# Kernel tuning notes

Hardware: AMD Instinct MI355X
Metric: run time of the kernel (lower is better)

Reference implementation:

```python
import jax, jax.numpy as jnp
import numpy as np

D_MODEL = 512
NUM_HEADS = 8
D_QKV = D_MODEL // NUM_HEADS  # 64
CAPACITY = 2  # EUNN tunable-style rotation layers per step
B = 2
L = 256


def setup_inputs() -> dict:
    key = jax.random.key(0)
    ks = jax.random.split(key, 16)
    f = jnp.float32
    x_q = jax.random.normal(ks[0], (B, L, D_MODEL), f)
    x_k = jax.random.normal(ks[1], (B, L, D_MODEL), f)
    x_v = jax.random.normal(ks[2], (B, L, D_MODEL), f)
    mask = jnp.zeros((B, 1, L, L), f)
    s = 1.0 / np.sqrt(D_MODEL).astype(np.float32)
    Wq = jax.random.normal(ks[3], (D_MODEL, D_MODEL), f) * s
    Wk = jax.random.normal(ks[4], (D_MODEL, D_MODEL), f) * s
    Wv = jax.random.normal(ks[5], (D_MODEL, D_MODEL), f) * s
    Wo = jax.random.normal(ks[6], (D_MODEL, D_MODEL), f) * s
    bq = jnp.zeros((D_MODEL,), f); bk = jnp.zeros((D_MODEL,), f)
    bv = jnp.zeros((D_MODEL,), f); bo = jnp.zeros((D_MODEL,), f)
    pi = np.float32(np.pi)
    theta = jax.random.uniform(ks[7], (NUM_HEADS, CAPACITY, D_QKV // 2), f, -pi, pi)
    phi = jax.random.uniform(ks[8], (NUM_HEADS, CAPACITY, D_QKV // 2), f, -pi, pi)
    sw = 1.0 / np.sqrt(D_QKV).astype(np.float32)
    Win_re = jax.random.normal(ks[9], (NUM_HEADS, D_QKV, D_QKV), f) * sw
    Win_im = jax.random.normal(ks[10], (NUM_HEADS, D_QKV, D_QKV), f) * sw
    rnn_bias = jax.random.normal(ks[11], (NUM_HEADS, D_QKV), f) * 0.01
    return dict(x_q=x_q, x_k=x_k, x_v=x_v, mask=mask, Wq=Wq, bq=bq, Wk=Wk, bk=bk,
                Wv=Wv, bv=bv, Wo=Wo, bo=bo, theta=theta, phi=phi,
                Win_re=Win_re, Win_im=Win_im, rnn_bias=rnn_bias)


def _apply_unitary(h, theta, phi):
    # h: [B,H,Q,d] complex64. EUNN unitary = product of Givens-rotation layers,
    # alternating even pairings (0,1),(2,3),.. and odd pairings via roll.
    for c in range(theta.shape[1]):
        if c % 2 == 1:
            h = jnp.roll(h, -1, axis=-1)
        sh = h.shape
        hp = h.reshape(sh[:-1] + (sh[-1] // 2, 2))
        a, b = hp[..., 0], hp[..., 1]
        cs = jnp.cos(theta[:, c, :])[None, :, None, :]
        sn = jnpp_sin = jnp.sin(theta[:, c, :])[None, :, None, :]
        ph = jnp.exp(1j * phi[:, c, :].astype(jnp.complex64))[None, :, None, :]
        na = cs * a - (sn * ph) * b
        nb = (sn * jnp.conj(ph)) * a + cs * b
        h = jnp.stack([na, nb], axis=-1).reshape(sh)
        if c % 2 == 1:
            h = jnp.roll(h, 1, axis=-1)
    return h


def _modrelu(z, b):
    m = jnp.abs(z)
    scale = jax.nn.relu(m + b) / (m + 1e-5)
    return z * scale.astype(z.dtype)


def _forward(x_q, x_k, x_v, mask, Wq, bq, Wk, bk, Wv, bv, Wo, bo,
             theta, phi, Win_re, Win_im, rnn_bias):
    Bm, Lq, _ = x_q.shape
    def heads(x):
        return x.reshape(Bm, -1, NUM_HEADS, D_QKV).transpose(0, 2, 1, 3)
    q = heads(x_q @ Wq + bq)   # [B,H,Lq,d]
    k = heads(x_k @ Wk + bk)   # [B,H,Lk,d]
    v = heads(x_v @ Wv + bv)   # [B,H,Lk,d]
    logits = jnp.einsum('bhqd,bhkd->bhqk', q, k) / jnp.sqrt(jnp.float32(D_QKV))
    logits = logits - jnp.where(mask == 1.0, jnp.inf, mask)
    attn = jax.nn.softmax(logits, axis=-1)  # [B,H,Lq,Lk]
    Win = (Win_re + 1j * Win_im).astype(jnp.complex64)  # [H,d,d]
    bb = rnn_bias[None, :, None, :]
    def step(h, xs):
        a_t, v_t = xs                              # [B,H,Q], [B,H,d]
        x_t = a_t[..., None] * v_t[:, :, None, :]  # [B,H,Q,d] streamed weighted value
        wx = jnp.einsum('bhqd,hde->bhqe', x_t.astype(jnp.complex64), Win)
        return _modrelu(_apply_unitary(h, theta, phi) + wx, bb), None
    h0 = jnp.zeros((Bm, NUM_HEADS, Lq, D_QKV), jnp.complex64)
    xs = (attn.transpose(3, 0, 1, 2), v.transpose(2, 0, 1, 3))
    hT, _ = jax.lax.scan(step, h0, xs)
    rnn_out = jnp.real(hT)  # [B,H,Lq,d] -- TF takes final RNN state, real part
    out = rnn_out.transpose(0, 2, 1, 3).reshape(Bm, Lq, D_MODEL) @ Wo + bo
    return out, attn


def reference(x_q, x_k, x_v, mask, Wq, bq, Wk, bk, Wv, bv, Wo, bo,
              theta, phi, Win_re, Win_im, rnn_bias):
    return _forward(x_q, x_k, x_v, mask, Wq, bq, Wk, bk, Wv, bv, Wo, bo,
                    theta, phi, Win_re, Win_im, rnn_bias)
```

## Files before the change

### kernel.cpp

```cpp
#include <hip/hip_runtime.h>
#include <math.h>

#define NB 2
#define NL 256
#define DM 512
#define NH 8
#define DQ 64

__global__ __launch_bounds__(256) void qkv_gemm(
    const float* __restrict__ xq, const float* __restrict__ xk,
    const float* __restrict__ xv,
    const float* __restrict__ Wq, const float* __restrict__ Wk,
    const float* __restrict__ Wv,
    const float* __restrict__ bq, const float* __restrict__ bk,
    const float* __restrict__ bv,
    float* __restrict__ q, float* __restrict__ k, float* __restrict__ v)
{
    int z = blockIdx.z;
    const float* X = (z == 0) ? xq : (z == 1) ? xk : xv;
    const float* W = (z == 0) ? Wq : (z == 1) ? Wk : Wv;
    const float* bias = (z == 0) ? bq : (z == 1) ? bk : bv;
    float* O = (z == 0) ? q : (z == 1) ? k : v;

    __shared__ float As[32][33];
    __shared__ float Bs[32][68];

    int tid = threadIdx.x;
    int tx = tid & 15, ty = tid >> 4;
    int m0 = blockIdx.y * 32, n0 = blockIdx.x * 64;

    float acc[2][4] = {};

    for (int k0 = 0; k0 < 512; k0 += 32) {
        {
            int r = tid >> 3, c4 = (tid & 7) * 4;
            const float4 av = *(const float4*)(X + (m0 + r) * 512 + k0 + c4);
            As[c4 + 0][r] = av.x; As[c4 + 1][r] = av.y;
            As[c4 + 2][r] = av.z; As[c4 + 3][r] = av.w;
        }
        {
            int r = tid >> 4, c4 = (tid & 15) * 4;
            float4 b0 = *(const float4*)(W + (k0 + r) * 512 + n0 + c4);
            float4 b1 = *(const float4*)(W + (k0 + r + 16) * 512 + n0 + c4);
            *(float4*)&Bs[r][c4] = b0;
            *(float4*)&Bs[r + 16][c4] = b1;
        }
        __syncthreads();
        #pragma unroll
        for (int kk = 0; kk < 32; kk++) {
            float a0 = As[kk][ty * 2 + 0];
            float a1 = As[kk][ty * 2 + 1];
            float4 bb = *(const float4*)&Bs[kk][tx * 4];
            acc[0][0] += a0 * bb.x; acc[0][1] += a0 * bb.y;
            acc[0][2] += a0 * bb.z; acc[0][3] += a0 * bb.w;
            acc[1][0] += a1 * bb.x; acc[1][1] += a1 * bb.y;
            acc[1][2] += a1 * bb.z; acc[1][3] += a1 * bb.w;
        }
        __syncthreads();
    }

    #pragma unroll
    for (int i = 0; i < 2; i++) {
        int m = m0 + ty * 2 + i;
        int b = m >> 8, l = m & 255;
        #pragma unroll
        for (int j = 0; j < 4; j++) {
            int n = n0 + tx * 4 + j;
            int h = n >> 6, d = n & 63;
            float val = acc[i][j] + bias[n];
            if (z == 1)
                O[((b * NH + h) * DQ + d) * NL + l] = val;
            else
                O[((b * NH + h) * NL + l) * DQ + d] = val;
        }
    }
}

__global__ __launch_bounds__(256) void attn_u_kernel(
    const float* __restrict__ q, const float* __restrict__ kT,
    const float* __restrict__ mask, float* __restrict__ attn_o,
    const float* __restrict__ v, const float* __restrict__ Wre,
    const float* __restrict__ Wim, float2* __restrict__ u)
{
    int h = blockIdx.y, b = blockIdx.z;
    int tid = threadIdx.x;
    int x = blockIdx.x;
    __shared__ float sp[2608];

    if (x < 32) {
        int qg = x;
        int wv = tid >> 6, lane = tid & 63;
        float* qs   = sp;
        float* lg   = sp + 512;
        float* redm = sp + 512 + 2080;
        float* reds = redm + 8;

        ((float2*)qs)[tid] =
            ((const float2*)(q + ((size_t)(b * NH + h) * NL + qg * 8) * DQ))[tid];
        __syncthreads();

        const float* kp = kT + (size_t)((b * NH + h) * DQ) * NL + tid;
        float acc[8] = {};
        #pragma unroll
        for (int d4 = 0; d4 < 16; d4++) {
            float kv0 = kp[(d4 * 4 + 0) * NL];
            float kv1 = kp[(d4 * 4 + 1) * NL];
            float kv2 = kp[(d4 * 4 + 2) * NL];
            float kv3 = kp[(d4 * 4 + 3) * NL];
            #pragma unroll
            for (int j = 0; j < 8; j++) {
                const float4 qv = *(const float4*)&qs[j * 64 + d4 * 4];
                acc[j] += qv.x * kv0 + qv.y * kv1 + qv.z * kv2 + qv.w * kv3;
            }
        }
        #pragma unroll
        for (int j = 0; j < 8; j++) {
            float mv = mask[(size_t)(b * NL + qg * 8 + j) * NL + tid];
            acc[j] = acc[j] * 0.125f - ((mv == 1.0f) ? INFINITY : mv);
            lg[j * 260 + tid] = acc[j];
        }
        __syncthreads();
        #pragma unroll
        for (int jj = 0; jj < 2; jj++) {
            int j = wv * 2 + jj;
            float v0 = lg[j * 260 + lane],       v1 = lg[j * 260 + 64 + lane];
            float v2 = lg[j * 260 + 128 + lane], v3 = lg[j * 260 + 192 + lane];
            float mx = fmaxf(fmaxf(v0, v1), fmaxf(v2, v3));
            #pragma unroll
            for (int o = 32; o; o >>= 1) mx = fmaxf(mx, __shfl_xor(mx, o, 64));
            float s = __expf(v0 - mx) + __expf(v1 - mx) +
                      __expf(v2 - mx) + __expf(v3 - mx);
            #pragma unroll
            for (int o = 32; o; o >>= 1) s += __shfl_xor(s, o, 64);
            if (lane == 0) { redm[j] = mx; reds[j] = s; }
        }
        __syncthreads();
        #pragma unroll
        for (int j = 0; j < 8; j++) {
            float p = __expf(acc[j] - redm[j]) * __builtin_amdgcn_rcpf(reds[j]);
            attn_o[((size_t)(b * NH + h) * NL + qg * 8 + j) * NL + tid] = p;
        }
    } else {
        int xi = x - 32;
        int e = tid & 63, tq = tid >> 6;
        int t = xi * 4 + tq;
        float (*vrow)[64] = (float (*)[64])sp;

        vrow[tq][e] = v[((b * NH + h) * NL + t) * DQ + e];
        __syncthreads();

        const float* wr = Wre + h * 4096 + e;
        const float* wi = Wim + h * 4096 + e;
        float ar = 0.f, ai = 0.f;
        #pragma unroll
        for (int d = 0; d < 64; d++) {
            float vv = vrow[tq][d];
            ar += vv * wr[d * 64];
            ai += vv * wi[d * 64];
        }
        u[((b * NH + h) * NL + t) * DQ + e] = make_float2(ar, ai);
    }
}

__device__ __forceinline__ float rot_up2(float x) {
    int v = __builtin_amdgcn_mov_dpp(__float_as_int(x), 0x134, 0xF, 0xF, true);
    v = __builtin_amdgcn_mov_dpp(v, 0x134, 0xF, 0xF, true);
    return __int_as_float(v);
}
__device__ __forceinline__ float rot_dn2(float x) {
    int v = __builtin_amdgcn_mov_dpp(__float_as_int(x), 0x13C, 0xF, 0xF, true);
    v = __builtin_amdgcn_mov_dpp(v, 0x13C, 0xF, 0xF, true);
    return __int_as_float(v);
}

__global__ __launch_bounds__(256) void rnn_kernel(
    const float* __restrict__ attn_f, const float2* __restrict__ u,
    const float* __restrict__ theta, const float* __restrict__ phi,
    const float* __restrict__ rnn_bias, float* __restrict__ rnn_out)
{
    int tid = threadIdx.x;
    int wv = tid >> 6;
    int lane = tid & 63;
    int par = lane & 1;
    int p = lane >> 1;
    int rec = blockIdx.x * 8 + wv * 2 + par;
    int qi = rec & 255, h = (rec >> 8) & 7, b = rec >> 11;

    const float* tb = theta + h * 64;
    const float* pb = phi + h * 64;

    float th0 = tb[p], ph0 = pb[p];
    float c0 = cosf(th0), s0 = sinf(th0);
    float cp0 = cosf(ph0), sp0 = sinf(ph0);
    float W0ar = -s0 * cp0, W0ai = -s0 * sp0;
    float W0br =  s0 * cp0, W0bi = -s0 * sp0;

    float th1 = tb[32 + p], ph1 = pb[32 + p];
    float c1 = cosf(th1), s1 = sinf(th1);
    float W1ar = -s1 * cosf(ph1), W1ai = -s1 * sinf(ph1);

    int pm = (p + 31) & 31;
    float th1m = tb[32 + pm], ph1m = pb[32 + pm];
    float c1m = cosf(th1m), s1m = sinf(th1m);
    float W1br = s1m * cosf(ph1m), W1bi = -s1m * sinf(ph1m);

    float bias0 = rnn_bias[h * 64 + 2 * p];
    float bias1 = rnn_bias[h * 64 + 2 * p + 1];

    __shared__ float arow[8 * 256];
    {
        const float4* ap = (const float4*)(attn_f + (size_t)blockIdx.x * 8 * 256);
        ((float4*)arow)[tid] = ap[tid];
        ((float4*)arow)[tid + 256] = ap[tid + 256];
    }
    __syncthreads();
    const float* arc = arow + (wv * 2 + par) * 256;

    const float4* up4 = (const float4*)(u + (size_t)((b * NH + h) * NL) * DQ) + p;

    float e0r = 0.f, e0i = 0.f, e1r = 0.f, e1i = 0.f;
    #pragma unroll 8
    for (int t = 0; t < 256; t++) {
        float4 uu = up4[t * 32];
        float a_t = arc[t];

        float na_r = c0 * e0r + (W0ar * e1r - W0ai * e1i);
        float na_i = c0 * e0i + (W0ar * e1i + W0ai * e1r);
        float nb_r = c0 * e1r + (W0br * e0r - W0bi * e0i);
        float nb_i = c0 * e1i + (W0br * e0i + W0bi * e0r);

        float f1r = rot_up2(na_r), f1i = rot_up2(na_i);
        float f2r = rot_dn2(nb_r), f2i = rot_dn2(nb_i);

        float z1r = c1 * nb_r + (W1ar * f1r - W1ai * f1i);
        float z1i = c1 * nb_i + (W1ar * f1i + W1ai * f1r);
        float z0r = c1m * na_r + (W1br * f2r - W1bi * f2i);
        float z0i = c1m * na_i + (W1br * f2i + W1bi * f2r);

        z0r += a_t * uu.x; z0i += a_t * uu.y;
        z1r += a_t * uu.z; z1i += a_t * uu.w;

        float mm0 = z0r * z0r + z0i * z0i;
        float m0 = __builtin_amdgcn_sqrtf(mm0);
        float sc0 = fmaxf(m0 + bias0, 0.f) * __builtin_amdgcn_rcpf(m0 + 1e-5f);
        e0r = z0r * sc0; e0i = z0i * sc0;

        float mm1 = z1r * z1r + z1i * z1i;
        float m1 = __builtin_amdgcn_sqrtf(mm1);
        float sc1 = fmaxf(m1 + bias1, 0.f) * __builtin_amdgcn_rcpf(m1 + 1e-5f);
        e1r = z1r * sc1; e1i = z1i * sc1;
    }

    float2 o = make_float2(e0r, e1r);
    *(float2*)&rnn_out[(size_t)(b * NL + qi) * DM + h * DQ + 2 * p] = o;
}

__global__ __launch_bounds__(256) void out_gemm(
    const float* __restrict__ A, const float* __restrict__ W,
    const float* __restrict__ bias, float* __restrict__ C)
{
    __shared__ float As[32][17];
    __shared__ float Bs[32][68];

    int tid = threadIdx.x;
    int tx = tid & 15, ty = tid >> 4;
    int m0 = blockIdx.y * 16, n0 = blockIdx.x * 64;

    float acc[4] = {};

    for (int k0 = 0; k0 < 512; k0 += 32) {
        {
            int r = tid >> 4, c2 = (tid & 15) * 2;
            const float2 av = *(const float2*)(A + (m0 + r) * 512 + k0 + c2);
            As[c2 + 0][r] = av.x; As[c2 + 1][r] = av.y;
        }
        {
            int r = tid >> 4, c4 = (tid & 15) * 4;
            float4 b0 = *(const float4*)(W + (k0 + r) * 512 + n0 + c4);
            float4 b1 = *(const float4*)(W + (k0 + r + 16) * 512 + n0 + c4);
            *(float4*)&Bs[r][c4] = b0;
            *(float4*)&Bs[r + 16][c4] = b1;
        }
        __syncthreads();
        #pragma unroll
        for (int kk = 0; kk < 32; kk++) {
            float a = As[kk][ty];
            float4 bb = *(const float4*)&Bs[kk][tx * 4];
            acc[0] += a * bb.x; acc[1] += a * bb.y;
            acc[2] += a * bb.z; acc[3] += a * bb.w;
        }
        __syncthreads();
    }

    int m = m0 + ty;
    #pragma unroll
    for (int j = 0; j < 4; j++) {
        int n = n0 + tx * 4 + j;
        C[m * 512 + n] = acc[j] + bias[n];
    }
}

extern "C" void kernel_launch(void* const* d_in, const int* in_sizes, int n_in,
                              void* d_out, int out_size, void* d_ws, size_t ws_size,
                              hipStream_t stream)
{
    const float* x_q  = (const float*)d_in[0];
    const float* x_k  = (const float*)d_in[1];
    const float* x_v  = (const float*)d_in[2];
    const float* mask = (const float*)d_in[3];
    const float* Wq   = (const float*)d_in[4];
    const float* bq   = (const float*)d_in[5];
    const float* Wk   = (const float*)d_in[6];
    const float* bk   = (const float*)d_in[7];
    const float* Wv   = (const float*)d_in[8];
    const float* bv   = (const float*)d_in[9];
    const float* Wo   = (const float*)d_in[10];
    const float* bo   = (const float*)d_in[11];
    const float* theta= (const float*)d_in[12];
    const float* phi  = (const float*)d_in[13];
    const float* Wre  = (const float*)d_in[14];
    const float* Wim  = (const float*)d_in[15];
    const float* rb   = (const float*)d_in[16];

    float* ws = (float*)d_ws;
    float*  q_ws    = ws;
    float*  kT_ws   = ws + 262144;
    float*  v_ws    = ws + 524288;
    float2* u_ws    = (float2*)(ws + 786432);
    float*  rnn_o   = ws + 1310720;

    float* out_o  = (float*)d_out;
    float* attn_o = out_o + NB * NL * DM;

    qkv_gemm<<<dim3(8, 16, 3), 256, 0, stream>>>(
        x_q, x_k, x_v, Wq, Wk, Wv, bq, bk, bv, q_ws, kT_ws, v_ws);

    attn_u_kernel<<<dim3(96, NH, NB), 256, 0, stream>>>(
        q_ws, kT_ws, mask, attn_o, v_ws, Wre, Wim, u_ws);

    rnn_kernel<<<dim3(512), 256, 0, stream>>>(
        attn_o, u_ws, theta, phi, rb, rnn_o);

    out_gemm<<<dim3(8, 32), 256, 0, stream>>>(rnn_o, Wo, bo, out_o);
}
```

Before: 195.8 us.

## Fuse complex input projection into V GEMM epilogue and vectorize RNN step

The V-projection blocks of the QKV GEMM now stage their output tile in shared memory and immediately multiply by the per-head complex input weights, writing u directly. This removes the intermediate v buffer and the separate u-computation blocks from the attention kernel, which now only runs the softmax blocks. The RNN inner loop is rewritten with float2 fma helpers, which may let the compiler emit packed FMAs on the serial critical path. In exchange, the V-GEMM blocks carry a longer epilogue that reads Win from global memory per block.

```diff
diff --git a/kernel.cpp b/kernel.cpp
--- a/kernel.cpp
+++ b/kernel.cpp
@@ -14,13 +14,13 @@
     const float* __restrict__ Wv,
     const float* __restrict__ bq, const float* __restrict__ bk,
     const float* __restrict__ bv,
-    float* __restrict__ q, float* __restrict__ k, float* __restrict__ v)
+    const float* __restrict__ Wre, const float* __restrict__ Wim,
+    float* __restrict__ q, float* __restrict__ kT, float2* __restrict__ u)
 {
     int z = blockIdx.z;
     const float* X = (z == 0) ? xq : (z == 1) ? xk : xv;
     const float* W = (z == 0) ? Wq : (z == 1) ? Wk : Wv;
     const float* bias = (z == 0) ? bq : (z == 1) ? bk : bv;
-    float* O = (z == 0) ? q : (z == 1) ? k : v;
 
     __shared__ float As[32][33];
     __shared__ float Bs[32][68];
@@ -59,106 +59,122 @@
         __syncthreads();
     }
 
-    #pragma unroll
-    for (int i = 0; i < 2; i++) {
-        int m = m0 + ty * 2 + i;
-        int b = m >> 8, l = m & 255;
-        #pragma unroll
-        for (int j = 0; j < 4; j++) {
-            int n = n0 + tx * 4 + j;
-            int h = n >> 6, d = n & 63;
-            float val = acc[i][j] + bias[n];
-            if (z == 1)
-                O[((b * NH + h) * DQ + d) * NL + l] = val;
-            else
-                O[((b * NH + h) * NL + l) * DQ + d] = val;
-        }
-    }
-}
-
-__global__ __launch_bounds__(256) void attn_u_kernel(
+    if (z < 2) {
+        float* O = (z == 0) ? q : kT;
+        #pragma unroll
+        for (int i = 0; i < 2; i++) {
+            int m = m0 + ty * 2 + i;
+            int b = m >> 8, l = m & 255;
+            #pragma unroll
+            for (int j = 0; j < 4; j++) {
+                int n = n0 + tx * 4 + j;
+                int h = n >> 6, d = n & 63;
+                float val = acc[i][j] + bias[n];
+                if (z == 1)
+                    O[((b * NH + h) * DQ + d) * NL + l] = val;
+                else
+                    O[((b * NH + h) * NL + l) * DQ + d] = val;
+            }
+        }
+    } else {
+        int h = blockIdx.x;
+        int b = m0 >> 8;
+        #pragma unroll
+        for (int i = 0; i < 2; i++)
+            #pragma unroll
+            for (int j = 0; j < 4; j++)
+                Bs[ty * 2 + i][tx * 4 + j] = acc[i][j] + bias[n0 + tx * 4 + j];
+        __syncthreads();
+
+        int r0 = ty * 2, c4 = tx * 4;
+        float ur[2][4] = {}, ui[2][4] = {};
+        const float* wr = Wre + h * 4096 + c4;
+        const float* wi = Wim + h * 4096 + c4;
+        #pragma unroll 4
+        for (int d = 0; d < 64; d++) {
+            float v0 = Bs[r0][d];
+            float v1 = Bs[r0 + 1][d];
+            float4 wre = *(const float4*)(wr + d * 64);
+            float4 wim = *(const float4*)(wi + d * 64);
+            ur[0][0] += v0 * wre.x; ur[0][1] += v0 * wre.y;
+            ur[0][2] += v0 * wre.z; ur[0][3] += v0 * wre.w;
+            ui[0][0] += v0 * wim.x; ui[0][1] += v0 * wim.y;
+            ui[0][2] += v0 * wim.z; ui[0][3] += v0 * wim.w;
+            ur[1][0] += v1 * wre.x; ur[1][1] += v1 * wre.y;
+            ur[1][2] += v1 * wre.z; ur[1][3] += v1 * wre.w;
+            ui[1][0] += v1 * wim.x; ui[1][1] += v1 * wim.y;
+            ui[1][2] += v1 * wim.z; ui[1][3] += v1 * wim.w;
+        }
+        #pragma unroll
+        for (int i = 0; i < 2; i++) {
+            int l = (m0 & 255) + r0 + i;
+            float2* up = u + ((size_t)(b * NH + h) * NL + l) * DQ + c4;
+            #pragma unroll
+            for (int j = 0; j < 4; j++)
+                up[j] = make_float2(ur[i][j], ui[i][j]);
+        }
+    }
+}
+
+__global__ __launch_bounds__(256) void attn_kernel(
     const float* __restrict__ q, const float* __restrict__ kT,
-    const float* __restrict__ mask, float* __restrict__ attn_o,
-    const float* __restrict__ v, const float* __restrict__ Wre,
-    const float* __restrict__ Wim, float2* __restrict__ u)
+    const float* __restrict__ mask, float* __restrict__ attn_o)
 {
     int h = blockIdx.y, b = blockIdx.z;
     int tid = threadIdx.x;
-    int x = blockIdx.x;
+    int qg = blockIdx.x;
     __shared__ float sp[2608];
 
-    if (x < 32) {
-        int qg = x;
-        int wv = tid >> 6, lane = tid & 63;
-        float* qs   = sp;
-        float* lg   = sp + 512;
-        float* redm = sp + 512 + 2080;
-        float* reds = redm + 8;
-
-        ((float2*)qs)[tid] =
-            ((const float2*)(q + ((size_t)(b * NH + h) * NL + qg * 8) * DQ))[tid];
-        __syncthreads();
-
-        const float* kp = kT + (size_t)((b * NH + h) * DQ) * NL + tid;
-        float acc[8] = {};
-        #pragma unroll
-        for (int d4 = 0; d4 < 16; d4++) {
-            float kv0 = kp[(d4 * 4 + 0) * NL];
-            float kv1 = kp[(d4 * 4 + 1) * NL];
-            float kv2 = kp[(d4 * 4 + 2) * NL];
-            float kv3 = kp[(d4 * 4 + 3) * NL];
-            #pragma unroll
-            for (int j = 0; j < 8; j++) {
-                const float4 qv = *(const float4*)&qs[j * 64 + d4 * 4];
-                acc[j] += qv.x * kv0 + qv.y * kv1 + qv.z * kv2 + qv.w * kv3;
-            }
-        }
+    int wv = tid >> 6, lane = tid & 63;
+    float* qs   = sp;
+    float* lg   = sp + 512;
+    float* redm = sp + 512 + 2080;
+    float* reds = redm + 8;
+
+    ((float2*)qs)[tid] =
+        ((const float2*)(q + ((size_t)(b * NH + h) * NL + qg * 8) * DQ))[tid];
+    __syncthreads();
+
+    const float* kp = kT + (size_t)((b * NH + h) * DQ) * NL + tid;
+    float acc[8] = {};
+    #pragma unroll
+    for (int d4 = 0; d4 < 16; d4++) {
+        float kv0 = kp[(d4 * 4 + 0) * NL];
+        float kv1 = kp[(d4 * 4 + 1) * NL];
+        float kv2 = kp[(d4 * 4 + 2) * NL];
+        float kv3 = kp[(d4 * 4 + 3) * NL];
         #pragma unroll
         for (int j = 0; j < 8; j++) {
-            float mv = mask[(size_t)(b * NL + qg * 8 + j) * NL + tid];
-            acc[j] = acc[j] * 0.125f - ((mv == 1.0f) ? INFINITY : mv);
-            lg[j * 260 + tid] = acc[j];
-        }
-        __syncthreads();
-        #pragma unroll
-        for (int jj = 0; jj < 2; jj++) {
-            int j = wv * 2 + jj;
-            float v0 = lg[j * 260 + lane],       v1 = lg[j * 260 + 64 + lane];
-            float v2 = lg[j * 260 + 128 + lane], v3 = lg[j * 260 + 192 + lane];
-            float mx = fmaxf(fmaxf(v0, v1), fmaxf(v2, v3));
-            #pragma unroll
-            for (int o = 32; o; o >>= 1) mx = fmaxf(mx, __shfl_xor(mx, o, 64));
-            float s = __expf(v0 - mx) + __expf(v1 - mx) +
-                      __expf(v2 - mx) + __expf(v3 - mx);
-            #pragma unroll
-            for (int o = 32; o; o >>= 1) s += __shfl_xor(s, o, 64);
-            if (lane == 0) { redm[j] = mx; reds[j] = s; }
-        }
-        __syncthreads();
-        #pragma unroll
-        for (int j = 0; j < 8; j++) {
-            float p = __expf(acc[j] - redm[j]) * __builtin_amdgcn_rcpf(reds[j]);
-            attn_o[((size_t)(b * NH + h) * NL + qg * 8 + j) * NL + tid] = p;
-        }
-    } else {
-        int xi = x - 32;
-        int e = tid & 63, tq = tid >> 6;
-        int t = xi * 4 + tq;
-        float (*vrow)[64] = (float (*)[64])sp;
-
-        vrow[tq][e] = v[((b * NH + h) * NL + t) * DQ + e];
-        __syncthreads();
-
-        const float* wr = Wre + h * 4096 + e;
-        const float* wi = Wim + h * 4096 + e;
-        float ar = 0.f, ai = 0.f;
-        #pragma unroll
-        for (int d = 0; d < 64; d++) {
-            float vv = vrow[tq][d];
-            ar += vv * wr[d * 64];
-            ai += vv * wi[d * 64];
-        }
-        u[((b * NH + h) * NL + t) * DQ + e] = make_float2(ar, ai);
+            const float4 qv = *(const float4*)&qs[j * 64 + d4 * 4];
+            acc[j] += qv.x * kv0 + qv.y * kv1 + qv.z * kv2 + qv.w * kv3;
+        }
+    }
+    #pragma unroll
+    for (int j = 0; j < 8; j++) {
+        float mv = mask[(size_t)(b * NL + qg * 8 + j) * NL + tid];
+        acc[j] = acc[j] * 0.125f - ((mv == 1.0f) ? INFINITY : mv);
+        lg[j * 260 + tid] = acc[j];
+    }
+    __syncthreads();
+    #pragma unroll
+    for (int jj = 0; jj < 2; jj++) {
+        int j = wv * 2 + jj;
+        float v0 = lg[j * 260 + lane],       v1 = lg[j * 260 + 64 + lane];
+        float v2 = lg[j * 260 + 128 + lane], v3 = lg[j * 260 + 192 + lane];
+        float mx = fmaxf(fmaxf(v0, v1), fmaxf(v2, v3));
+        #pragma unroll
+        for (int o = 32; o; o >>= 1) mx = fmaxf(mx, __shfl_xor(mx, o, 64));
+        float s = __expf(v0 - mx) + __expf(v1 - mx) +
+                  __expf(v2 - mx) + __expf(v3 - mx);
+        #pragma unroll
+        for (int o = 32; o; o >>= 1) s += __shfl_xor(s, o, 64);
+        if (lane == 0) { redm[j] = mx; reds[j] = s; }
+    }
+    __syncthreads();
+    #pragma unroll
+    for (int j = 0; j < 8; j++) {
+        float p = __expf(acc[j] - redm[j]) * __builtin_amdgcn_rcpf(reds[j]);
+        attn_o[((size_t)(b * NH + h) * NL + qg * 8 + j) * NL + tid] = p;
     }
 }
 
@@ -171,6 +187,15 @@
     int v = __builtin_amdgcn_mov_dpp(__float_as_int(x), 0x13C, 0xF, 0xF, true);
     v = __builtin_amdgcn_mov_dpp(v, 0x13C, 0xF, 0xF, true);
     return __int_as_float(v);
+}
+__device__ __forceinline__ float2 fma2(float s, float2 a, float2 b) {
+    return make_float2(fmaf(s, a.x, b.x), fmaf(s, a.y, b.y));
+}
+__device__ __forceinline__ float2 mul2(float s, float2 a) {
+    return make_float2(s * a.x, s * a.y);
+}
+__device__ __forceinline__ float2 rot90(float2 a) {
+    return make_float2(-a.y, a.x);
 }
 
 __global__ __launch_bounds__(256) void rnn_kernel(
@@ -218,41 +243,36 @@
 
     const float4* up4 = (const float4*)(u + (size_t)((b * NH + h) * NL) * DQ) + p;
 
-    float e0r = 0.f, e0i = 0.f, e1r = 0.f, e1i = 0.f;
+    float2 e0 = make_float2(0.f, 0.f), e1 = make_float2(0.f, 0.f);
     #pragma unroll 8
     for (int t = 0; t < 256; t++) {
         float4 uu = up4[t * 32];
         float a_t = arc[t];
 
-        float na_r = c0 * e0r + (W0ar * e1r - W0ai * e1i);
-        float na_i = c0 * e0i + (W0ar * e1i + W0ai * e1r);
-        float nb_r = c0 * e1r + (W0br * e0r - W0bi * e0i);
-        float nb_i = c0 * e1i + (W0br * e0i + W0bi * e0r);
-
-        float f1r = rot_up2(na_r), f1i = rot_up2(na_i);
-        float f2r = rot_dn2(nb_r), f2i = rot_dn2(nb_i);
-
-        float z1r = c1 * nb_r + (W1ar * f1r - W1ai * f1i);
-        float z1i = c1 * nb_i + (W1ar * f1i + W1ai * f1r);
-        float z0r = c1m * na_r + (W1br * f2r - W1bi * f2i);
-        float z0i = c1m * na_i + (W1br * f2i + W1bi * f2r);
-
-        z0r += a_t * uu.x; z0i += a_t * uu.y;
-        z1r += a_t * uu.z; z1i += a_t * uu.w;
-
-        float mm0 = z0r * z0r + z0i * z0i;
+        float2 na = fma2(c0, e0, fma2(W0ar, e1, mul2(W0ai, rot90(e1))));
+        float2 nb = fma2(c0, e1, fma2(W0br, e0, mul2(W0bi, rot90(e0))));
+
+        float2 f1 = make_float2(rot_up2(na.x), rot_up2(na.y));
+        float2 f2 = make_float2(rot_dn2(nb.x), rot_dn2(nb.y));
+
+        float2 z1 = fma2(a_t, make_float2(uu.z, uu.w),
+                     fma2(c1, nb, fma2(W1ar, f1, mul2(W1ai, rot90(f1)))));
+        float2 z0 = fma2(a_t, make_float2(uu.x, uu.y),
+                     fma2(c1m, na, fma2(W1br, f2, mul2(W1bi, rot90(f2)))));
+
+        float mm0 = z0.x * z0.x + z0.y * z0.y;
         float m0 = __builtin_amdgcn_sqrtf(mm0);
         float sc0 = fmaxf(m0 + bias0, 0.f) * __builtin_amdgcn_rcpf(m0 + 1e-5f);
-        e0r = z0r * sc0; e0i = z0i * sc0;
-
-        float mm1 = z1r * z1r + z1i * z1i;
+        e0 = mul2(sc0, z0);
+
+        float mm1 = z1.x * z1.x + z1.y * z1.y;
         float m1 = __builtin_amdgcn_sqrtf(mm1);
         float sc1 = fmaxf(m1 + bias1, 0.f) * __builtin_amdgcn_rcpf(m1 + 1e-5f);
-        e1r = z1r * sc1; e1i = z1i * sc1;
-    }
-
-    float2 o = make_float2(e0r, e1r);
-    *(float2*)&rnn_out[(size_t)(b * NL + qi) * DM + h * DQ + 2 * p] = o;
+        e1 = mul2(sc1, z1);
+    }
+
+    *(float2*)&rnn_out[(size_t)(b * NL + qi) * DM + h * DQ + 2 * p] =
+        make_float2(e0.x, e1.x);
 }
 
 __global__ __launch_bounds__(256) void out_gemm(
@@ -325,18 +345,18 @@
     float* ws = (float*)d_ws;
     float*  q_ws    = ws;
     float*  kT_ws   = ws + 262144;
-    float*  v_ws    = ws + 524288;
-    float2* u_ws    = (float2*)(ws + 786432);
-    float*  rnn_o   = ws + 1310720;
+    float2* u_ws    = (float2*)(ws + 524288);
+    float*  rnn_o   = ws + 1048576;
 
     float* out_o  = (float*)d_out;
     float* attn_o = out_o + NB * NL * DM;
 
     qkv_gemm<<<dim3(8, 16, 3), 256, 0, stream>>>(
-        x_q, x_k, x_v, Wq, Wk, Wv, bq, bk, bv, q_ws, kT_ws, v_ws);
-
-    attn_u_kernel<<<dim3(96, NH, NB), 256, 0, stream>>>(
-        q_ws, kT_ws, mask, attn_o, v_ws, Wre, Wim, u_ws);
+        x_q, x_k, x_v, Wq, Wk, Wv, bq, bk, bv, Wre, Wim,
+        q_ws, kT_ws, u_ws);
+
+    attn_kernel<<<dim3(32, NH, NB), 256, 0, stream>>>(
+        q_ws, kT_ws, mask, attn_o);
 
     rnn_kernel<<<dim3(512), 256, 0, stream>>>(
         attn_o, u_ws, theta, phi, rb, rnn_o);
```

Result: slower. 203.5 us (+3.9%).
